# Kernel optimization log

Measured on AMD Instinct MI355X. Metric: run time of the kernel, lower is better.

Reference implementation:

```python
import jax, jax.numpy as jnp
import numpy as np

B, S, D, H = 4, 2048, 1024, 16
HD = D // H  # head_dim = 64


def setup_inputs() -> dict:
    key = jax.random.key(0)
    ks = jax.random.split(key, 5)
    scale = 0.02
    x = jax.random.normal(ks[0], (B, S, D), dtype=jnp.float32)
    Wq = jax.random.normal(ks[1], (D, D), dtype=jnp.float32) * scale
    Wk = jax.random.normal(ks[2], (D, D), dtype=jnp.float32) * scale
    Wv = jax.random.normal(ks[3], (D, D), dtype=jnp.float32) * scale
    Wo = jax.random.normal(ks[4], (D, D), dtype=jnp.float32) * scale
    # causal mask, broadcastable [1,1,S,S]; 0 entries get -10000 like masked_fill
    mask = jnp.tril(jnp.ones((S, S), dtype=jnp.int32))[None, None]
    return {"x": x, "Wq": Wq, "Wk": Wk, "Wv": Wv, "Wo": Wo, "mask": mask}


def reference(x, Wq, Wk, Wv, Wo, mask):
    b, s, _ = x.shape
    # nn.Linear: x @ W.T (no bias)
    q = (x @ Wq.T).reshape(b, s, H, HD).transpose(0, 2, 1, 3)  # [B,H,S,HD]
    k = (x @ Wk.T).reshape(b, s, H, HD).transpose(0, 2, 1, 3)
    v = (x @ Wv.T).reshape(b, s, H, HD).transpose(0, 2, 1, 3)
    attn = jnp.einsum('bhqd,bhkd->bhqk', q, k) / (HD ** 0.5)  # [B,H,S,S]
    attn = jnp.where(mask == 0, jnp.float32(-10000.0), attn)
    attn = jax.nn.softmax(attn, axis=-1)
    out = jnp.einsum('bhqk,bhkd->bhqd', attn, v)  # [B,H,S,HD]
    out = out.transpose(0, 2, 1, 3).reshape(b, s, H * HD)
    return out @ Wo.T
```

## Files before the change

kernel.cpp:

```cpp
#include <hip/hip_runtime.h>

typedef float    f4 __attribute__((ext_vector_type(4)));
typedef _Float16 h8 __attribute__((ext_vector_type(8)));
typedef _Float16 h4 __attribute__((ext_vector_type(4)));
typedef _Float16 h2 __attribute__((ext_vector_type(2)));
typedef unsigned u4 __attribute__((ext_vector_type(4)));

#define DEV static __device__ __forceinline__

DEV f4 mfma16(h8 a, h8 b, f4 c) {
  return __builtin_amdgcn_mfma_f32_16x16x32_f16(a, b, c, 0, 0, 0);
}

DEV void gload16(const void* g, void* lds) {
  __builtin_amdgcn_global_load_lds((__attribute__((address_space(1))) void*)g,
                                   (__attribute__((address_space(3))) void*)lds,
                                   16, 0, 0);
}

DEV unsigned cvtpku(float a, float b) {
  return __builtin_bit_cast(unsigned, __builtin_amdgcn_cvt_pkrtz(a, b));
}

DEV float max3f(float a, float b, float c) {
  float d;
  asm("v_max3_f32 %0, %1, %2, %3" : "=v"(d) : "v"(a), "v"(b), "v"(c));
  return d;
}

__global__ __launch_bounds__(256) void cvt_all(
    const float* __restrict__ x,  const float* __restrict__ wq,
    const float* __restrict__ wk, const float* __restrict__ wv,
    const float* __restrict__ wo,
    _Float16* __restrict__ xb, _Float16* __restrict__ wqkv, _Float16* __restrict__ wob)
{
  int b = blockIdx.x;
  const float* src; _Float16* dst; int i4;
  if      (b < 8192)  { src = x;  dst = xb;                 i4 = b * 256; }
  else if (b < 9216)  { src = wq; dst = wqkv;               i4 = (b - 8192)  * 256; }
  else if (b < 10240) { src = wk; dst = wqkv + (1u << 20);  i4 = (b - 9216)  * 256; }
  else if (b < 11264) { src = wv; dst = wqkv + (2u << 20);  i4 = (b - 10240) * 256; }
  else                { src = wo; dst = wob;                i4 = (b - 11264) * 256; }
  i4 += threadIdx.x;
  f4 v = ((const f4*)src)[i4];
  h4 o;
  o[0] = (_Float16)v[0]; o[1] = (_Float16)v[1];
  o[2] = (_Float16)v[2]; o[3] = (_Float16)v[3];
  ((h4*)dst)[i4] = o;
}

template<int MODE, int MF, int NF>
__global__ __launch_bounds__(512) void gemmT(
    const _Float16* __restrict__ A, const _Float16* __restrict__ Bt,
    float* __restrict__ C,
    _Float16* __restrict__ Qo, _Float16* __restrict__ Ko, _Float16* __restrict__ Vo,
    int N, int Nt)
{
  constexpr int ASZ = MF * 16 * 64;
  constexpr int BSZ = NF * 32 * 64;
  constexpr int ALD = (MF == 8) ? 2 : 1;
  constexpr int BLD = NF / 2;
  constexpr int L   = 2 * (ALD + BLD);
  constexpr int V1  = (3 * L) / 2;
  constexpr int V2  = 3 * ALD + 2 * BLD;
  constexpr int VL3 = L;
  constexpr int VL5 = L / 2;
  constexpr int VL6 = L - ALD - 2 * BLD;
  __shared__ _Float16 Al[4 * ASZ];
  __shared__ _Float16 Bl[4 * BSZ];

  int bid = blockIdx.x;
  int cpx = gridDim.x >> 3;
  bid = (bid & 7) * cpx + (bid >> 3);
  int tm = bid / Nt, tn = bid - tm * Nt;
  int m0 = tm * (MF * 32), n0 = tn * (NF * 64);

  int t = threadIdx.x, w = t >> 6, l = t & 63, lo = l & 15, hi = l >> 4;
  int wm = w >> 2, wn = w & 3;

  int rsc = t >> 3;
  int csrc = ((t & 7) ^ (rsc & 7)) * 8;
  const _Float16 *As[2][2], *Bs[2][2];
  #pragma unroll
  for (int q = 0; q < 2; ++q) {
    if (MF == 8) {
      As[q][0] = A + (size_t)(m0 + q * 64 + rsc) * 1024 + csrc;
      As[q][1] = A + (size_t)(m0 + 128 + q * 64 + rsc) * 1024 + csrc;
    } else {
      As[q][0] = A + (size_t)(m0 + (t >> 8) * 64 + q * 32 + (rsc & 31)) * 1024 + csrc;
      As[q][1] = As[q][0];
    }
    #pragma unroll
    for (int h = 0; h < 2; ++h) {
      if (NF == 4)
        Bs[q][h] = Bt + (size_t)(n0 + (2 * h + (t >> 8)) * 64 + q * 32 + (rsc & 31)) * 1024 + csrc;
      else
        Bs[q][h] = Bt + (size_t)(n0 + (rsc >> 4) * 32 + q * 16 + (rsc & 15)) * 1024 + csrc;
    }
  }
  _Float16* Adst = Al + w * 512;
  _Float16* Bdst = Bl + w * 512;

  int awoff = wm * (MF * 8 * 64) + lo * 64;
  int bwoff = wn * (NF * 512) + lo * 64;
  int s0 = (hi ^ (lo & 7)) * 8;
  int s1 = ((4 + hi) ^ (lo & 7)) * 8;

  f4 acc[MF][NF] = {};
  h8 ar[MF / 2][2], br[2][NF / 2][2];

#define VMW(n)  asm volatile("s_waitcnt vmcnt(%0)" :: "n"(n) : "memory")
#define BARR    __builtin_amdgcn_s_barrier()
#define LGKM0   do { asm volatile("s_waitcnt lgkmcnt(0)" ::: "memory"); \
                     __builtin_amdgcn_sched_barrier(0); } while (0)
#define STA(BUF, Q, KO) do { \
    gload16(As[Q][0] + (KO), Adst + ((BUF) * 2 + (Q)) * ASZ); \
    if (MF == 8) gload16(As[Q][1] + (KO), Adst + ((BUF) * 2 + (Q)) * ASZ + 4096); \
  } while (0)
#define STB(BUF, QN, KO) do { \
    gload16(Bs[QN][0] + (KO), Bdst + ((BUF) * 2 + (QN)) * BSZ); \
    if (NF == 4) gload16(Bs[QN][1] + (KO), Bdst + ((BUF) * 2 + (QN)) * BSZ + 4096); \
  } while (0)
#define RDA(BUF, Q) do { \
    const _Float16* p_ = Al + ((BUF) * 2 + (Q)) * ASZ + awoff; \
    _Pragma("unroll") \
    for (int f_ = 0; f_ < MF / 2; ++f_) { \
      ar[f_][0] = *(const h8*)(p_ + f_ * 1024 + s0); \
      ar[f_][1] = *(const h8*)(p_ + f_ * 1024 + s1); } \
  } while (0)
#define RDB(BUF, QN, D) do { \
    const _Float16* p_ = Bl + ((BUF) * 2 + (QN)) * BSZ + bwoff; \
    _Pragma("unroll") \
    for (int g_ = 0; g_ < NF / 2; ++g_) { \
      br[D][g_][0] = *(const h8*)(p_ + g_ * 1024 + s0); \
      br[D][g_][1] = *(const h8*)(p_ + g_ * 1024 + s1); } \
  } while (0)
#define MM(MH, D) do { \
    __builtin_amdgcn_s_setprio(1); \
    _Pragma("unroll") \
    for (int f_ = 0; f_ < MF / 2; ++f_) \
      _Pragma("unroll") \
      for (int g_ = 0; g_ < NF / 2; ++g_) { \
        acc[(MH) * (MF / 2) + f_][(D) * (NF / 2) + g_] = \
            mfma16(ar[f_][0], br[D][g_][0], acc[(MH) * (MF / 2) + f_][(D) * (NF / 2) + g_]); \
        acc[(MH) * (MF / 2) + f_][(D) * (NF / 2) + g_] = \
            mfma16(ar[f_][1], br[D][g_][1], acc[(MH) * (MF / 2) + f_][(D) * (NF / 2) + g_]); } \
    __builtin_amdgcn_s_setprio(0); \
    __builtin_amdgcn_sched_barrier(0); \
  } while (0)

  STA(0, 0, 0);  STB(0, 0, 0);  STB(0, 1, 0);  STA(0, 1, 0);
  STA(1, 0, 64); STB(1, 0, 64); STB(1, 1, 64); STA(1, 1, 64);

  int kof = 128;
  #pragma unroll 1
  for (int it = 0; it < 7; ++it) {
    VMW(V1); BARR; RDA(0, 0); RDB(0, 0, 0); LGKM0; MM(0, 0);
    VMW(V2); BARR; RDB(0, 1, 1); STA(0, 0, kof); STB(0, 0, kof); LGKM0; MM(0, 1);
    VMW(V1); BARR; RDA(0, 1); STB(0, 1, kof); LGKM0; MM(1, 1);
    BARR; STA(0, 1, kof); MM(1, 0);
    VMW(V1); BARR; RDA(1, 0); RDB(1, 0, 0); LGKM0; MM(0, 0);
    VMW(V2); BARR; RDB(1, 1, 1); STA(1, 0, kof + 64); STB(1, 0, kof + 64); LGKM0; MM(0, 1);
    VMW(V1); BARR; RDA(1, 1); STB(1, 1, kof + 64); LGKM0; MM(1, 1);
    BARR; STA(1, 1, kof + 64); MM(1, 0);
    kof += 128;
  }
  VMW(V1);  BARR; RDA(0, 0); RDB(0, 0, 0); LGKM0; MM(0, 0);
  VMW(V2);  BARR; RDB(0, 1, 1); LGKM0; MM(0, 1);
  VMW(VL3); BARR; RDA(0, 1); LGKM0; MM(1, 1);
  BARR; MM(1, 0);
  VMW(VL5); BARR; RDA(1, 0); RDB(1, 0, 0); LGKM0; MM(0, 0);
  VMW(VL6); BARR; RDB(1, 1, 1); LGKM0; MM(0, 1);
  VMW(0);   BARR; RDA(1, 1); LGKM0; MM(1, 1);
  BARR; MM(1, 0);

#undef VMW
#undef BARR
#undef LGKM0
#undef STA
#undef STB
#undef RDA
#undef RDB
#undef MM

  if (MODE == 0) {
    #pragma unroll
    for (int mi = 0; mi < MF; ++mi)
      #pragma unroll
      for (int nf = 0; nf < NF; ++nf)
        #pragma unroll
        for (int j = 0; j < 4; ++j) {
          int row = m0 + wm * (MF * 16) + mi * 16 + hi * 4 + j;
          int col = n0 + wn * (NF * 16) + nf * 16 + lo;
          C[(size_t)row * N + col] = acc[mi][nf][j];
        }
  } else {
    int which = n0 >> 10;
    int cb0 = (n0 & 1023) + wn * (NF * 16);
    if (which == 2) {
      #pragma unroll
      for (int mi = 0; mi < MF; ++mi) {
        int row0 = m0 + wm * (MF * 16) + mi * 16 + hi * 4;
        int bb = row0 >> 11, ss0 = row0 & 2047;
        #pragma unroll
        for (int nf = 0; nf < NF; ++nf) {
          int col = cb0 + nf * 16 + lo;
          int hh = col >> 6, hd = col & 63;
          h4 o4;
          o4[0] = (_Float16)acc[mi][nf][0]; o4[1] = (_Float16)acc[mi][nf][1];
          o4[2] = (_Float16)acc[mi][nf][2]; o4[3] = (_Float16)acc[mi][nf][3];
          *(h4*)(Vo + (size_t)(bb * 16 + hh) * 131072 + (size_t)hd * 2048 + ss0) = o4;
        }
      }
    } else {
      _Float16* Dst = (which == 0) ? Qo : Ko;
      float qs = (which == 0) ? 0.1803368801111137f : 1.0f;
      #pragma unroll
      for (int mi = 0; mi < MF; ++mi)
        #pragma unroll
        for (int nf = 0; nf < NF; ++nf)
          #pragma unroll
          for (int j = 0; j < 4; ++j) {
            int row = m0 + wm * (MF * 16) + mi * 16 + hi * 4 + j;
            int col = cb0 + nf * 16 + lo;
            int hh = col >> 6, hd = col & 63;
            int bb = row >> 11, ss = row & 2047;
            Dst[(size_t)(bb * 16 + hh) * 131072 + (size_t)ss * 64 + hd] =
                (_Float16)(acc[mi][nf][j] * qs);
          }
    }
  }
}

__global__ __launch_bounds__(512, 4) void attn_kernel(
    const _Float16* __restrict__ Q, const _Float16* __restrict__ Kb,
    const _Float16* __restrict__ Vb, _Float16* __restrict__ O)
{
  __shared__ _Float16 Kl[2 * 4096];
  __shared__ _Float16 Vl[2 * 4096];

  int bid = blockIdx.x;
  int bh = bid & 63, qi = 15 - (bid >> 6);
  int t = threadIdx.x, w = t >> 6, l = t & 63, lo = l & 15, hi = l >> 4;
  const size_t hoff = (size_t)bh * 131072;
  const _Float16* Kg = Kb + hoff;
  const _Float16* Vg = Vb + hoff;
  int bb = bh >> 4, hh = bh & 15;

  int rs = t >> 3, cs = t & 7;
  int sw_ = (cs ^ (rs & 7)) * 8;
  int sigma = ((rs & 0x1C) << 1) | (rs & 3) | ((rs & 32) >> 3);
  int srcK = sigma * 64 + sw_;
  int srcV = rs * 2048 + sw_;
  _Float16* kd0 = Kl + w * 512;
  _Float16* vd0 = Vl + w * 512;

  int koff[4][2];
  #pragma unroll
  for (int kf = 0; kf < 4; ++kf) {
    int row = kf * 16 + lo;
    koff[kf][0] = row * 64 + ((hi       ^ (row & 7)) * 8);
    koff[kf][1] = row * 64 + (((4 + hi) ^ (row & 7)) * 8);
  }

  h8 ones;
  #pragma unroll
  for (int e = 0; e < 8; ++e) ones[e] = (_Float16)1.0f;

  int qb = qi * 128 + w * 16;
  const _Float16* Qp = Q + hoff + (size_t)(qb + lo) * 64 + hi * 8;
  h8 qf0 = *(const h8*)(Qp);
  h8 qf1 = *(const h8*)(Qp + 32);

  f4 acc[4] = {};
  float m_run = -1e30f, l_run = 0.f;
  int nkt = 2 * qi + 2;

#define STAGE(buf, kt) do {                                                   \
    const _Float16* Kt_ = Kg + (size_t)(kt) * 4096;                           \
    const _Float16* Vt_ = Vg + (size_t)(kt) * 64;                             \
    gload16(Kt_ + srcK, kd0 + (buf) * 4096);                                  \
    gload16(Vt_ + srcV, vd0 + (buf) * 4096);                                  \
  } while (0)

#define ITER(kt, buf) do {                                                    \
    if ((kt) + 1 < nkt) STAGE(buf ^ 1, (kt) + 1);                             \
    const _Float16* Kc = Kl + (buf) * 4096;                                   \
    const _Float16* Vc = Vl + (buf) * 4096;                                   \
    f4 sc[4] = {};                                                            \
    __builtin_amdgcn_s_setprio(1);                                            \
    _Pragma("unroll")                                                         \
    for (int kf = 0; kf < 4; ++kf) {                                          \
      h8 k0 = *(const h8*)(Kc + koff[kf][0]);                                 \
      h8 k1 = *(const h8*)(Kc + koff[kf][1]);                                 \
      sc[kf] = mfma16(k0, qf0, sc[kf]);                                       \
      sc[kf] = mfma16(k1, qf1, sc[kf]);                                       \
    }                                                                         \
    __builtin_amdgcn_s_setprio(0);                                            \
    if ((kt) >= 2 * qi) {                                                     \
      int qg = qb + lo;                                                       \
      _Pragma("unroll")                                                       \
      for (int kf = 0; kf < 4; ++kf) {                                        \
        int kgb = (kt) * 64 + ((kf & 1) << 5) + ((kf >> 1) << 2) + hi * 8;    \
        _Pragma("unroll")                                                     \
        for (int j = 0; j < 4; ++j)                                           \
          if (kgb + j > qg) sc[kf][j] = -1e30f;                               \
      }                                                                       \
    }                                                                         \
    {                                                                         \
      f4 m4;                                                                  \
      _Pragma("unroll")                                                       \
      for (int c = 0; c < 4; ++c)                                             \
        m4[c] = fmaxf(max3f(sc[0][c], sc[1][c], sc[2][c]), sc[3][c]);         \
      float mx = fmaxf(max3f(m4[0], m4[1], m4[2]), m4[3]);                    \
      if (!__all(mx <= m_run + 8.f)) {              \
        mx = fmaxf(mx, __shfl_xor(mx, 16));                                   \
        mx = fmaxf(mx, __shfl_xor(mx, 32));                                   \
        float mn = fmaxf(m_run, mx);                                          \
        float cr = exp2f(m_run - mn);                                         \
        m_run = mn;                                                           \
        l_run *= cr;                                                          \
        _Pragma("unroll")                                                     \
        for (int df = 0; df < 4; ++df) {                                      \
          acc[df][0] *= cr; acc[df][1] *= cr;                                 \
          acc[df][2] *= cr; acc[df][3] *= cr;                                 \
        }                                                                     \
      }                                                                       \
    }                                                                         \
    f4 ls = {};                                                               \
    _Pragma("unroll")                                                         \
    for (int ks = 0; ks < 2; ++ks) {                                          \
      u4 tw;                                                                  \
      tw[0] = cvtpku(exp2f(sc[ks    ][0] - m_run),                            \
                     exp2f(sc[ks    ][1] - m_run));                           \
      tw[1] = cvtpku(exp2f(sc[ks    ][2] - m_run),                            \
                     exp2f(sc[ks    ][3] - m_run));                           \
      tw[2] = cvtpku(exp2f(sc[2 + ks][0] - m_run),                            \
                     exp2f(sc[2 + ks][1] - m_run));                           \
      tw[3] = cvtpku(exp2f(sc[2 + ks][2] - m_run),                            \
                     exp2f(sc[2 + ks][3] - m_run));                           \
      h8 pf = __builtin_bit_cast(h8, tw);                                     \
      ls = mfma16(ones, pf, ls);                                              \
      __builtin_amdgcn_s_setprio(1);                                          \
      _Pragma("unroll")                                                       \
      for (int df = 0; df < 4; ++df) {                                        \
        h8 vf = *(const h8*)(Vc + koff[df][ks]);                              \
        acc[df] = mfma16(vf, pf, acc[df]);                                    \
      }                                                                       \
      __builtin_amdgcn_s_setprio(0);                                          \
    }                                                                         \
    l_run += ls[0];                                                           \
    asm volatile("s_waitcnt vmcnt(0)" ::: "memory");                          \
    __syncthreads();                                                          \
  } while (0)

  STAGE(0, 0);
  asm volatile("s_waitcnt vmcnt(0)" ::: "memory");
  __syncthreads();

  for (int kt = 0; kt < nkt; kt += 2) {
    ITER(kt, 0);
    ITER(kt + 1, 1);
  }

  {
    float inv = 1.0f / l_run;
    int q = qb + lo;
    _Float16* Op = O + ((size_t)(bb * 2048 + q)) * 1024 + hh * 64 + (hi << 2);
    #pragma unroll
    for (int df = 0; df < 4; ++df) {
      h4 o4;
      o4[0] = (_Float16)(acc[df][0] * inv);
      o4[1] = (_Float16)(acc[df][1] * inv);
      o4[2] = (_Float16)(acc[df][2] * inv);
      o4[3] = (_Float16)(acc[df][3] * inv);
      *(h4*)(Op + df * 16) = o4;
    }
  }
#undef ITER
#undef STAGE
}

extern "C" void kernel_launch(void* const* d_in, const int* in_sizes, int n_in,
                              void* d_out, int out_size, void* d_ws, size_t ws_size,
                              hipStream_t stream)
{
  const float* x  = (const float*)d_in[0];
  const float* wq = (const float*)d_in[1];
  const float* wk = (const float*)d_in[2];
  const float* wv = (const float*)d_in[3];
  const float* wo = (const float*)d_in[4];

  char* ws = (char*)d_ws;
  _Float16* xb   = (_Float16*)(ws);
  _Float16* wqkv = (_Float16*)(ws + (16u << 20));
  _Float16* wob  = (_Float16*)(ws + (22u << 20));
  _Float16* Qb   = (_Float16*)(ws + (24u << 20));
  _Float16* Kb   = (_Float16*)(ws + (40u << 20));
  _Float16* Vb   = (_Float16*)(ws + (56u << 20));
  _Float16* Ob   = xb;

  cvt_all<<<12288, 256, 0, stream>>>(x, wq, wk, wv, wo, xb, wqkv, wob);
  gemmT<1, 8, 4><<<32 * 12, 512, 0, stream>>>(xb, wqkv, nullptr, Qb, Kb, Vb, 3072, 12);
  attn_kernel<<<1024, 512, 0, stream>>>(Qb, Kb, Vb, Ob);
  gemmT<0, 4, 2><<<64 * 8, 512, 0, stream>>>(Ob, wob, (float*)d_out,
                                             nullptr, nullptr, nullptr, 1024, 8);
}
```

Baseline: 161.0 us.

## Restructure GEMM main loop to coarse per-half-tile vmcnt waits with ping-pong barriers

Replaces the fine-grained per-phase vmcnt waits in the GEMM K-loop with a single full wait for outstanding global-to-LDS loads at the end of each half-iteration. Barriers now bracket every MFMA phase, as in a ping-pong schedule between waves. The aim is a simpler, more regular interleaving of LDS reads, global loads and MFMAs across warps. In exchange it adds roughly twice as many barriers and waits for whole tiles instead of individual loads, which may expose more memory latency.

```diff
diff --git a/kernel.cpp b/kernel.cpp
--- a/kernel.cpp
+++ b/kernel.cpp
@@ -61,11 +61,6 @@
   constexpr int ALD = (MF == 8) ? 2 : 1;
   constexpr int BLD = NF / 2;
   constexpr int L   = 2 * (ALD + BLD);
-  constexpr int V1  = (3 * L) / 2;
-  constexpr int V2  = 3 * ALD + 2 * BLD;
-  constexpr int VL3 = L;
-  constexpr int VL5 = L / 2;
-  constexpr int VL6 = L - ALD - 2 * BLD;
   __shared__ _Float16 Al[4 * ASZ];
   __shared__ _Float16 Bl[4 * BSZ];
 
@@ -151,28 +146,29 @@
 
   STA(0, 0, 0);  STB(0, 0, 0);  STB(0, 1, 0);  STA(0, 1, 0);
   STA(1, 0, 64); STB(1, 0, 64); STB(1, 1, 64); STA(1, 1, 64);
+  VMW(L); BARR;
 
   int kof = 128;
   #pragma unroll 1
   for (int it = 0; it < 7; ++it) {
-    VMW(V1); BARR; RDA(0, 0); RDB(0, 0, 0); LGKM0; MM(0, 0);
-    VMW(V2); BARR; RDB(0, 1, 1); STA(0, 0, kof); STB(0, 0, kof); LGKM0; MM(0, 1);
-    VMW(V1); BARR; RDA(0, 1); STB(0, 1, kof); LGKM0; MM(1, 1);
-    BARR; STA(0, 1, kof); MM(1, 0);
-    VMW(V1); BARR; RDA(1, 0); RDB(1, 0, 0); LGKM0; MM(0, 0);
-    VMW(V2); BARR; RDB(1, 1, 1); STA(1, 0, kof + 64); STB(1, 0, kof + 64); LGKM0; MM(0, 1);
-    VMW(V1); BARR; RDA(1, 1); STB(1, 1, kof + 64); LGKM0; MM(1, 1);
-    BARR; STA(1, 1, kof + 64); MM(1, 0);
+    RDA(0, 0); RDB(0, 0, 0);                          BARR; LGKM0; MM(0, 0); BARR;
+    RDB(0, 1, 1); STA(0, 0, kof); STB(0, 0, kof);     BARR; LGKM0; MM(0, 1); BARR;
+    RDA(0, 1); STB(0, 1, kof);                        BARR; LGKM0; MM(1, 1); BARR;
+    STA(0, 1, kof); MM(1, 0); VMW(L);                 BARR;
+    RDA(1, 0); RDB(1, 0, 0);                          BARR; LGKM0; MM(0, 0); BARR;
+    RDB(1, 1, 1); STA(1, 0, kof + 64); STB(1, 0, kof + 64); BARR; LGKM0; MM(0, 1); BARR;
+    RDA(1, 1); STB(1, 1, kof + 64);                   BARR; LGKM0; MM(1, 1); BARR;
+    STA(1, 1, kof + 64); MM(1, 0); VMW(L);            BARR;
     kof += 128;
   }
-  VMW(V1);  BARR; RDA(0, 0); RDB(0, 0, 0); LGKM0; MM(0, 0);
-  VMW(V2);  BARR; RDB(0, 1, 1); LGKM0; MM(0, 1);
-  VMW(VL3); BARR; RDA(0, 1); LGKM0; MM(1, 1);
-  BARR; MM(1, 0);
-  VMW(VL5); BARR; RDA(1, 0); RDB(1, 0, 0); LGKM0; MM(0, 0);
-  VMW(VL6); BARR; RDB(1, 1, 1); LGKM0; MM(0, 1);
-  VMW(0);   BARR; RDA(1, 1); LGKM0; MM(1, 1);
-  BARR; MM(1, 0);
+  RDA(0, 0); RDB(0, 0, 0);  BARR; LGKM0; MM(0, 0); BARR;
+  RDB(0, 1, 1);             BARR; LGKM0; MM(0, 1); BARR;
+  RDA(0, 1);                BARR; LGKM0; MM(1, 1); BARR;
+  MM(1, 0); VMW(0);         BARR;
+  RDA(1, 0); RDB(1, 0, 0);  BARR; LGKM0; MM(0, 0); BARR;
+  RDB(1, 1, 1);             BARR; LGKM0; MM(0, 1); BARR;
+  RDA(1, 1);                BARR; LGKM0; MM(1, 1); BARR;
+  MM(1, 0);
 
 #undef VMW
 #undef BARR
```

New measurement: 164.6 us. 1.02x slower.
